# Kernel optimization log

Hardware: AMD Instinct MI355X
Metric: run time of the kernel (lower is better)

The kernel has to match this reference:

```python
import jax, jax.numpy as jnp
import numpy as np

N = 400_000      # total nodes in batched graph
E = 6_400_000    # total edges (avg degree 16)
G = 6_400        # total small graphs
B = 64           # samples; num[i] graphs per sample, sum(num)=G
F = 31           # feature dim (hard-coded in TAG)
K = 2            # TAGConv hops
L = 5            # number of TAGConv layers
MAXG = 120       # max graphs per sample (120*31 pad)


def setup_inputs() -> dict:
    key = jax.random.key(0)
    ks = jax.random.split(key, 8)
    x = jax.random.normal(ks[0], (N, F), dtype=jnp.float32)
    src = jax.random.randint(ks[1], (E,), 0, N, dtype=jnp.int32)
    dst = jax.random.randint(ks[2], (E,), 0, N, dtype=jnp.int32)
    # contiguous (sorted) graph assignment, every graph non-empty (~62 nodes each)
    graph_ids = jnp.asarray((np.arange(N, dtype=np.int64) * G) // N, dtype=jnp.int32)
    num = jnp.full((B,), G // B, dtype=jnp.int32)  # 100 graphs per sample
    Ws = jax.random.normal(ks[3], (L, (K + 1) * F, F), dtype=jnp.float32) * 0.1
    bs = jax.random.normal(ks[4], (L, F), dtype=jnp.float32) * 0.01
    w_gate = jax.random.normal(ks[5], (F,), dtype=jnp.float32) * 0.1
    b_gate = jax.random.normal(ks[6], (1,), dtype=jnp.float32) * 0.01
    return {"x": x, "Ws": Ws, "bs": bs, "w_gate": w_gate, "b_gate": b_gate,
            "src": src, "dst": dst, "graph_ids": graph_ids, "num": num}


def reference(x, Ws, bs, w_gate, b_gate, src, dst, graph_ids, num):
    # symmetric normalization: norm = in_deg^{-1/2}, deg clamped to >=1 (DGL TAGConv)
    deg = jax.ops.segment_sum(jnp.ones((E,), x.dtype), dst, num_segments=N)
    norm = jnp.clip(deg, 1.0, None) ** -0.5  # [N]

    def tagconv(h, W, b):
        fstack = [h]
        cur = h
        for _ in range(K):
            cur = norm[:, None] * cur
            cur = jax.ops.segment_sum(cur[src], dst, num_segments=N)  # SPMM hop
            cur = norm[:, None] * cur
            fstack.append(cur)
        return jnp.concatenate(fstack, axis=-1) @ W + b  # [N, F]

    h = x
    for l in range(L):
        h = jax.nn.relu(tagconv(h, Ws[l], bs[l]))

    # GlobalAttentionPooling: segment softmax over gate scores, weighted sum
    gate = h @ w_gate + b_gate[0]                                   # [N]
    gmax = jax.ops.segment_max(gate, graph_ids, num_segments=G)     # [G]
    e = jnp.exp(gate - gmax[graph_ids])
    den = jax.ops.segment_sum(e, graph_ids, num_segments=G)
    alpha = e / den[graph_ids]
    rep = jax.ops.segment_sum(alpha[:, None] * h, graph_ids, num_segments=G)  # [G, F]

    # split by num, flatten, pad to 120*31, stack
    csum = jnp.cumsum(num)
    offsets = jnp.concatenate([jnp.zeros((1,), jnp.int32), csum.astype(jnp.int32)])
    g = jnp.arange(G, dtype=jnp.int32)
    sample_id = jnp.searchsorted(csum, g, side="right").astype(jnp.int32)  # [G]
    pos = g - offsets[sample_id]
    out = jnp.zeros((B, MAXG, F), rep.dtype).at[sample_id, pos].set(rep)
    return out.reshape(B, MAXG * F)
```

## Files before the change

kernel.cpp:

```cpp
#include <hip/hip_runtime.h>
#include <hip/hip_bf16.h>

#define FDIM 31
#define FPAD 32
#define RSTRIDE 16

#define CBITS 11
#define CW    (1 << CBITS)
#define MAXBUK 256
#define TILE 4096

typedef int      iv4 __attribute__((ext_vector_type(4)));
typedef unsigned uv4 __attribute__((ext_vector_type(4)));

__device__ __forceinline__ float bf_lo(unsigned u) { return __uint_as_float(u << 16); }
__device__ __forceinline__ float bf_hi(unsigned u) { return __uint_as_float(u & 0xFFFF0000u); }
__device__ __forceinline__ unsigned pack2(float lo, float hi) {
    unsigned a = __float_as_uint(lo), b = __float_as_uint(hi);
    unsigned ra = (a + 0x7FFFu + ((a >> 16) & 1u)) >> 16;
    unsigned rb = (b + 0x7FFFu + ((b >> 16) & 1u)) >> 16;
    return ra | (rb << 16);
}

__device__ __forceinline__ int lb_gid(const int* __restrict__ gid, int Ntot, int g) {
    int lo = 0, hi = Ntot;
    while (lo < hi) { int mid = (lo + hi) >> 1; if (gid[mid] < g) lo = mid + 1; else hi = mid; }
    return lo;
}

__global__ __launch_bounds__(256) void multisplit_kernel(
    const int* __restrict__ src, const int* __restrict__ dst,
    int* __restrict__ gcnt, int* __restrict__ bucketed,
    int cap, int E, int nbuk)
{
    __shared__ int ordered[TILE];
    __shared__ int hist[MAXBUK];
    __shared__ int lofs[MAXBUK + 1];
    __shared__ int base_[MAXBUK];
    __shared__ int cur[MAXBUK];
    const int tid = threadIdx.x;
    const int e0 = blockIdx.x * TILE;
    const int n = min(TILE, E - e0);
    if (tid < MAXBUK) hist[tid] = 0;
    __syncthreads();
    for (int i = tid; i < n; i += 256)
        atomicAdd(&hist[dst[e0 + i] >> CBITS], 1);
    __syncthreads();
    if (tid == 0) {
        int a = 0;
        for (int b = 0; b < nbuk; ++b) { lofs[b] = a; a += hist[b]; }
        lofs[nbuk] = a;
    }
    __syncthreads();
    if (tid < nbuk) {
        int h = hist[tid];
        base_[tid] = h ? atomicAdd(&gcnt[tid], h) : 0;
        cur[tid] = lofs[tid];
    }
    __syncthreads();
    for (int i = tid; i < n; i += 256) {
        int s = src[e0 + i], d = dst[e0 + i];
        int b = d >> CBITS;
        int r = atomicAdd(&cur[b], 1);
        ordered[r] = (s << CBITS) | (d & (CW - 1));
    }
    __syncthreads();
    for (int i = tid; i < n; i += 256) {
        int lo = 0, hi = nbuk;
        while (hi - lo > 1) {
            int mid = (lo + hi) >> 1;
            if (lofs[mid] <= i) lo = mid; else hi = mid;
        }
        int b = lo;
        int pos = base_[b] + (i - lofs[b]);
        if (pos < cap) bucketed[(size_t)b * cap + pos] = ordered[i];
    }
}

__global__ void small_scans_kernel(const int* __restrict__ num, int* __restrict__ soff, int Bn,
                                   const int* __restrict__ gcnt, int* __restrict__ bbase,
                                   int nbuk, int cap) {
    if (threadIdx.x == 0 && blockIdx.x == 0) {
        int acc = 0; soff[0] = 0;
        for (int i = 0; i < Bn; ++i) { acc += num[i]; soff[i + 1] = acc; }
        int a = 0;
        for (int b = 0; b < nbuk; ++b) {
            bbase[b] = a;
            a += ((min(gcnt[b], cap) + 7) & ~7) + 7 * CW;
        }
    }
}

__global__ __launch_bounds__(1024) void bucket_build_kernel(
    const int* __restrict__ bucketed, const int* __restrict__ gcnt,
    const int* __restrict__ bbase,
    int* __restrict__ rowbeg, int* __restrict__ rowend,
    float* __restrict__ normv, float* __restrict__ invn,
    int* __restrict__ col,
    int cap, int N, int nbuk)
{
    __shared__ int hist[CW];
    __shared__ int lcur[CW];
    const int b = blockIdx.x, tid = threadIdx.x;
    hist[tid] = 0; hist[tid + 1024] = 0;
    __syncthreads();
    const int cnt = min(gcnt[b], cap);
    const int* reg = bucketed + (size_t)b * cap;
    for (int i = tid; i < cnt; i += 1024)
        atomicAdd(&hist[reg[i] & (CW - 1)], 1);
    __syncthreads();
    int c0 = hist[tid], c1 = hist[tid + 1024];
    int p0 = (c0 + 7) & ~7, p1 = (c1 + 7) & ~7;
    __syncthreads();
    hist[tid] = p0; hist[tid + 1024] = p1;
    __syncthreads();
    for (int off = 1; off < CW; off <<= 1) {
        int a0 = (tid >= off) ? hist[tid - off] : 0;
        int a1 = (tid + 1024 >= off) ? hist[tid + 1024 - off] : 0;
        __syncthreads();
        hist[tid] += a0; hist[tid + 1024] += a1;
        __syncthreads();
    }
    const int base = bbase[b];
    const int base_node = b << CBITS;
    int r0 = -1, r1 = -1;
    int node = base_node + tid;
    if (node < N) {
        r0 = base + hist[tid] - p0;
        rowbeg[node] = r0; rowend[node] = r0 + p0; lcur[tid] = r0;
        int cr = c0 > 0 ? c0 : 1;
        normv[node] = rsqrtf((float)cr);
        invn[node]  = sqrtf((float)cr);
    }
    node = base_node + tid + 1024;
    if (node < N) {
        r1 = base + hist[tid + 1024] - p1;
        rowbeg[node] = r1; rowend[node] = r1 + p1; lcur[tid + 1024] = r1;
        int cr = c1 > 0 ? c1 : 1;
        normv[node] = rsqrtf((float)cr);
        invn[node]  = sqrtf((float)cr);
    }
    __syncthreads();
    for (int i = tid; i < cnt; i += 1024) {
        int e = reg[i];
        int p = atomicAdd(&lcur[e & (CW - 1)], 1);
        col[p] = e >> CBITS;
    }
    if (r0 >= 0) for (int j = r0 + c0; j < r0 + p0; ++j) col[j] = N;
    if (r1 >= 0) for (int j = r1 + c1; j < r1 + p1; ++j) col[j] = N;
}

__global__ void cast_x_kernel(const float* __restrict__ x, const float* __restrict__ normv,
                              unsigned* __restrict__ A, int N) {
    int idx = blockIdx.x * 256 + threadIdx.x;
    if (idx >= (N + 1) * RSTRIDE) return;
    int n = idx >> 4, q = idx & 15;
    if (n >= N) { A[idx] = 0u; return; }
    float nv = normv[n];
    int f0 = 2 * q, f1 = 2 * q + 1;
    float lo = (f0 < FDIM) ? nv * x[(size_t)n * FDIM + f0] : 0.0f;
    float hi = (f1 < FDIM) ? nv * x[(size_t)n * FDIM + f1] : 0.0f;
    A[idx] = pack2(lo, hi);
}

#define GATHER8(HSRC, r0, r1, r2, r3, r4, r5, r6, r7, CA, CB)                    \
    r0 = *((const uint4*)(HSRC + (size_t)(CA).x * RSTRIDE) + sub);               \
    r1 = *((const uint4*)(HSRC + (size_t)(CA).y * RSTRIDE) + sub);               \
    r2 = *((const uint4*)(HSRC + (size_t)(CA).z * RSTRIDE) + sub);               \
    r3 = *((const uint4*)(HSRC + (size_t)(CA).w * RSTRIDE) + sub);               \
    r4 = *((const uint4*)(HSRC + (size_t)(CB).x * RSTRIDE) + sub);               \
    r5 = *((const uint4*)(HSRC + (size_t)(CB).y * RSTRIDE) + sub);               \
    r6 = *((const uint4*)(HSRC + (size_t)(CB).z * RSTRIDE) + sub);               \
    r7 = *((const uint4*)(HSRC + (size_t)(CB).w * RSTRIDE) + sub);

#define ACC_EDGE(vN)                                                   \
    acc0 += bf_lo(vN.x); acc1 += bf_hi(vN.x);                          \
    acc2 += bf_lo(vN.y); acc3 += bf_hi(vN.y);                          \
    acc4 += bf_lo(vN.z); acc5 += bf_hi(vN.z);                          \
    acc6 += bf_lo(vN.w); acc7 += bf_hi(vN.w);

#define ACC8(r0, r1, r2, r3, r4, r5, r6, r7)                           \
    ACC_EDGE(r0) ACC_EDGE(r1) ACC_EDGE(r2) ACC_EDGE(r3)                \
    ACC_EDGE(r4) ACC_EDGE(r5) ACC_EDGE(r6) ACC_EDGE(r7)

__global__ __launch_bounds__(256) void spmm_kernel(const unsigned* __restrict__ Hin,
                                                   unsigned* __restrict__ Hout,
                                                   const int* __restrict__ rowbeg,
                                                   const int* __restrict__ rowend,
                                                   const int* __restrict__ col,
                                                   const float* __restrict__ normv, int N) {
    int node = blockIdx.x * 64 + (threadIdx.x >> 2);
    int sub = threadIdx.x & 3;
    if (node > N) return;
    if (node == N) {
        uint4 z; z.x = z.y = z.z = z.w = 0u;
        *((uint4*)(Hout + (size_t)N * RSTRIDE) + sub) = z;
        return;
    }
    int s = rowbeg[node];
    int nit = (rowend[node] - s) >> 3;
    float acc0 = 0.f, acc1 = 0.f, acc2 = 0.f, acc3 = 0.f;
    float acc4 = 0.f, acc5 = 0.f, acc6 = 0.f, acc7 = 0.f;
    if (nit > 0) {
        const iv4* cl = (const iv4*)(col + s);
        iv4 ca = __builtin_nontemporal_load(cl);
        iv4 cb = __builtin_nontemporal_load(cl + 1);
        for (int it = 0; it < nit; ++it) {
            uint4 v0, v1, v2, v3, v4, v5, v6, v7;
            GATHER8(Hin, v0, v1, v2, v3, v4, v5, v6, v7, ca, cb)
            const iv4* nx = cl + ((it + 1 < nit) ? 2 : 0);
            iv4 na = __builtin_nontemporal_load(nx);
            iv4 nb = __builtin_nontemporal_load(nx + 1);
            cl += 2;
            ACC8(v0, v1, v2, v3, v4, v5, v6, v7)
            ca = na; cb = nb;
        }
    }
    float nv = normv[node];
    float nn2 = nv * nv;
    uint4 o;
    o.x = pack2(nn2 * acc0, nn2 * acc1);
    o.y = pack2(nn2 * acc2, nn2 * acc3);
    o.z = pack2(nn2 * acc4, nn2 * acc5);
    o.w = pack2(nn2 * acc6, nn2 * acc7);
    *((uint4*)(Hout + (size_t)node * RSTRIDE) + sub) = o;
}

template<int JB, int NJ>
__device__ __forceinline__ void mlp_pre(const uint4 (&ra)[4], const uint4 (&rb)[4],
                                        const float* __restrict__ W, float (&out)[8]) {
    const unsigned* ru = (const unsigned*)ra;
    const unsigned* rv = (const unsigned*)rb;
#pragma unroll
    for (int i = 0; i < FDIM; ++i) {
        float va = (i & 1) ? bf_hi(ru[i >> 1]) : bf_lo(ru[i >> 1]);
        float vb = (i & 1) ? bf_hi(rv[i >> 1]) : bf_lo(rv[i >> 1]);
#pragma unroll
        for (int jj = 0; jj < NJ; ++jj) {
            out[jj] = fmaf(va, W[i * FDIM + JB + jj], out[jj]);
            out[jj] = fmaf(vb, W[FDIM * FDIM + i * FDIM + JB + jj], out[jj]);
        }
    }
}

template<int JB, int NJ>
__device__ __forceinline__ void mlp_fin(float (&out)[8], const float* hp,
                                        const float* __restrict__ W,
                                        const float* __restrict__ bias,
                                        float inv, float sc, unsigned* orow,
                                        const float* __restrict__ w_gate,
                                        int do_gate, float& gp) {
#pragma unroll
    for (int i = 0; i < FDIM; ++i) {
        float v = hp[i];
#pragma unroll
        for (int jj = 0; jj < NJ; ++jj)
            out[jj] = fmaf(v, W[2 * FDIM * FDIM + i * FDIM + JB + jj], out[jj]);
    }
#pragma unroll
    for (int jj = 0; jj < NJ; ++jj)
        out[jj] = fmaxf(fmaf(out[jj], inv, bias[JB + jj]), 0.0f);
#pragma unroll
    for (int jj = NJ; jj < 8; ++jj) out[jj] = 0.0f;
    uint4 q;
    q.x = pack2(sc * out[0], sc * out[1]);
    q.y = pack2(sc * out[2], sc * out[3]);
    q.z = pack2(sc * out[4], sc * out[5]);
    q.w = pack2(sc * out[6], sc * out[7]);
    ((uint4*)orow)[JB >> 3] = q;
    if (do_gate) {
#pragma unroll
        for (int jj = 0; jj < NJ; ++jj)
            gp = fmaf(out[jj], w_gate[JB + jj], gp);
    }
}

__global__ __launch_bounds__(256, 4) void spmm_mlp_kernel(
    const unsigned* __restrict__ Hb,
    unsigned* __restrict__ Ha,
    const int* __restrict__ rowbeg,
    const int* __restrict__ rowend,
    const int* __restrict__ col,
    const float* __restrict__ normv,
    const float* __restrict__ invn,
    const float* __restrict__ W,
    const float* __restrict__ bias,
    float* __restrict__ gatev,
    const float* __restrict__ w_gate,
    const float* __restrict__ b_gate,
    int do_gate, int N)
{
    __shared__ float hcL[64 * 33];
    __shared__ float gred[256];
    const int tid = threadIdx.x;
    const int ln = tid & 63;
    const int wv = tid >> 6;
    const int n2 = blockIdx.x * 64 + ln;
    uint4 ra[4], rb[4];
    if (n2 < N) {
        const uint4* pa = (const uint4*)(Ha + (size_t)n2 * RSTRIDE);
        const uint4* pb = (const uint4*)(Hb + (size_t)n2 * RSTRIDE);
#pragma unroll
        for (int q = 0; q < 4; ++q) ra[q] = pa[q];
#pragma unroll
        for (int q = 0; q < 4; ++q) rb[q] = pb[q];
    }
    {
        int node = blockIdx.x * 64 + (tid >> 2);
        int sub = tid & 3;
        if (node < N) {
            int s = rowbeg[node];
            int nit = (rowend[node] - s) >> 3;
            float acc0 = 0.f, acc1 = 0.f, acc2 = 0.f, acc3 = 0.f;
            float acc4 = 0.f, acc5 = 0.f, acc6 = 0.f, acc7 = 0.f;
            if (nit > 0) {
                const iv4* cl = (const iv4*)(col + s);
                iv4 ca = __builtin_nontemporal_load(cl);
                iv4 cb = __builtin_nontemporal_load(cl + 1);
                for (int it = 0; it < nit; ++it) {
                    uint4 v0, v1, v2, v3, v4, v5, v6, v7;
                    GATHER8(Hb, v0, v1, v2, v3, v4, v5, v6, v7, ca, cb)
                    const iv4* nx = cl + ((it + 1 < nit) ? 2 : 0);
                    iv4 na = __builtin_nontemporal_load(nx);
                    iv4 nb = __builtin_nontemporal_load(nx + 1);
                    cl += 2;
                    ACC8(v0, v1, v2, v3, v4, v5, v6, v7)
                    ca = na; cb = nb;
                }
            }
            float nv = normv[node];
            float nn2 = nv * nv;
            float* hp = &hcL[(tid >> 2) * 33 + sub * 8];
            hp[0] = nn2 * acc0; hp[1] = nn2 * acc1;
            hp[2] = nn2 * acc2; hp[3] = nn2 * acc3;
            hp[4] = nn2 * acc4; hp[5] = nn2 * acc5;
            hp[6] = nn2 * acc6; hp[7] = nn2 * acc7;
        }
    }
    float out[8];
#pragma unroll
    for (int jj = 0; jj < 8; ++jj) out[jj] = 0.0f;
    if (n2 < N) {
        if      (wv == 0) mlp_pre<0,  8>(ra, rb, W, out);
        else if (wv == 1) mlp_pre<8,  8>(ra, rb, W, out);
        else if (wv == 2) mlp_pre<16, 8>(ra, rb, W, out);
        else              mlp_pre<24, 7>(ra, rb, W, out);
    }
    __syncthreads();
    float gp = 0.0f;
    if (n2 < N) {
        const float* hp = &hcL[ln * 33];
        float inv = invn[n2];
        float sc = do_gate ? 1.0f : normv[n2];
        unsigned* orow = Ha + (size_t)n2 * RSTRIDE;
        if      (wv == 0) mlp_fin<0,  8>(out, hp, W, bias, inv, sc, orow, w_gate, do_gate, gp);
        else if (wv == 1) mlp_fin<8,  8>(out, hp, W, bias, inv, sc, orow, w_gate, do_gate, gp);
        else if (wv == 2) mlp_fin<16, 8>(out, hp, W, bias, inv, sc, orow, w_gate, do_gate, gp);
        else              mlp_fin<24, 7>(out, hp, W, bias, inv, sc, orow, w_gate, do_gate, gp);
    }
    if (do_gate) {
        gred[tid] = gp;
        __syncthreads();
        if (tid < 64 && n2 < N)
            gatev[n2] = b_gate[0] + gred[tid] + gred[tid + 64] + gred[tid + 128] + gred[tid + 192];
    }
}


__global__ __launch_bounds__(64) void graph_reduce_kernel(const float* __restrict__ gate,
                                                          const int* __restrict__ gid,
                                                          const int* __restrict__ soff, int Bn,
                                                          int Ntot,
                                                          float* __restrict__ gmax,
                                                          float* __restrict__ gden) {
    int g = blockIdx.x;
    if (g >= soff[Bn]) return;
    int s = lb_gid(gid, Ntot, g), e = lb_gid(gid, Ntot, g + 1);
    float m = -1e30f;
    for (int n = s + threadIdx.x; n < e; n += 64) m = fmaxf(m, gate[n]);
#pragma unroll
    for (int o = 32; o > 0; o >>= 1) m = fmaxf(m, __shfl_xor(m, o));
    float d = 0.0f;
    for (int n = s + threadIdx.x; n < e; n += 64) d += expf(gate[n] - m);
#pragma unroll
    for (int o = 32; o > 0; o >>= 1) d += __shfl_xor(d, o);
    if (threadIdx.x == 0) { gmax[g] = m; gden[g] = d; }
}

__global__ __launch_bounds__(64) void rep_scatter_kernel(const unsigned short* __restrict__ H,
                                                         const float* __restrict__ gate,
                                                         const int* __restrict__ gid,
                                                         const int* __restrict__ soff,
                                                         int MAXG, int Ntot,
                                                         const float* __restrict__ gmax,
                                                         const float* __restrict__ gden,
                                                         float* __restrict__ out) {
    int s = blockIdx.x / MAXG;
    int pos = blockIdx.x % MAXG;
    int t = threadIdx.x;
    if (t >= FDIM) return;
    int gbeg = soff[s], gend = soff[s + 1];
    float* op = out + ((size_t)s * MAXG + pos) * FDIM + t;
    if (pos >= gend - gbeg) { *op = 0.0f; return; }
    int g = gbeg + pos;
    int ns = lb_gid(gid, Ntot, g), ne = lb_gid(gid, Ntot, g + 1);
    float m = gmax[g], den = gden[g];
    float acc = 0.0f;
    for (int n = ns; n < ne; ++n) {
        float hv = __uint_as_float((unsigned)H[(size_t)n * FPAD + t] << 16);
        acc += expf(gate[n] - m) * hv;
    }
    *op = acc / den;
}


extern "C" void kernel_launch(void* const* d_in, const int* in_sizes, int n_in,
                              void* d_out, int out_size, void* d_ws, size_t ws_size,
                              hipStream_t stream) {
    const float* x      = (const float*)d_in[0];
    const float* Ws     = (const float*)d_in[1];
    const float* bs     = (const float*)d_in[2];
    const float* w_gate = (const float*)d_in[3];
    const float* b_gate = (const float*)d_in[4];
    const int* src       = (const int*)d_in[5];
    const int* dst       = (const int*)d_in[6];
    const int* graph_ids = (const int*)d_in[7];
    const int* num       = (const int*)d_in[8];
    float* out  = (float*)d_out;

    const int N  = in_sizes[7];
    const int E  = in_sizes[5];
    const int Bn = in_sizes[8];
    const int F  = in_sizes[3];
    const int L  = in_sizes[2] / F;
    const int nW = in_sizes[1];
    const int WperL = nW / L;
    const int MAXG = out_size / (Bn * F);
    const int Gmax = Bn * MAXG;

    const int nbuk = (N + CW - 1) / CW;
    const int cap  = E / nbuk + E / (8 * nbuk) + 2048;

    char* p = (char*)d_ws;
    auto alloc = [&](size_t bytes) {
        void* r = (void*)p;
        p += (bytes + 255) & ~(size_t)255;
        return r;
    };
    unsigned* HA = (unsigned*)alloc((size_t)(N + 1) * RSTRIDE * 4);
    unsigned* HB = (unsigned*)alloc((size_t)(N + 1) * RSTRIDE * 4);
    int*   colw  = (int*)alloc(((size_t)E + (size_t)nbuk * (7 * CW + 16)) * 4);
    int*   bkt   = (int*)alloc((size_t)nbuk * cap * 4);
    int*   gcnt  = (int*)alloc((size_t)nbuk * 4);
    int*   bbase = (int*)alloc((size_t)nbuk * 4);
    int*   rowb  = (int*)alloc((size_t)(N + 1) * 4);
    int*   rowe  = (int*)alloc((size_t)(N + 1) * 4);
    float* normv = (float*)alloc((size_t)N * 4);
    float* invnv = (float*)alloc((size_t)N * 4);
    float* gatev = (float*)alloc((size_t)N * 4);
    float* gmax  = (float*)alloc((size_t)Gmax * 4);
    float* gden  = (float*)alloc((size_t)Gmax * 4);
    int*   soff  = (int*)alloc((size_t)(Bn + 1) * 4);

    (void)hipMemsetAsync(gcnt, 0, (size_t)nbuk * 4, stream);

    const int NT = (E + TILE - 1) / TILE;
    multisplit_kernel<<<NT, 256, 0, stream>>>(src, dst, gcnt, bkt, cap, E, nbuk);
    small_scans_kernel<<<1, 64, 0, stream>>>(num, soff, Bn, gcnt, bbase, nbuk, cap);
    bucket_build_kernel<<<nbuk, 1024, 0, stream>>>(bkt, gcnt, bbase, rowb, rowe,
                                                   normv, invnv, colw, cap, N, nbuk);

    cast_x_kernel<<<((N + 1) * RSTRIDE + 255) / 256, 256, 0, stream>>>(x, normv, HA, N);

    const int SB  = (N + 1 + 63) / 64;
    const int SB2 = (N + 63) / 64;
    for (int l = 0; l < L; ++l) {
        spmm_kernel<<<SB, 256, 0, stream>>>(HA, HB, rowb, rowe, colw, normv, N);
        spmm_mlp_kernel<<<SB2, 256, 0, stream>>>(HB, HA, rowb, rowe, colw, normv, invnv,
                                                 Ws + (size_t)l * WperL, bs + (size_t)l * F,
                                                 gatev, w_gate, b_gate,
                                                 (l == L - 1) ? 1 : 0, N);
    }

    graph_reduce_kernel<<<Gmax, 64, 0, stream>>>(gatev, graph_ids, soff, Bn, N, gmax, gden);
    rep_scatter_kernel<<<Gmax, 64, 0, stream>>>((const unsigned short*)HA, gatev, graph_ids,
                                                soff, MAXG, N, gmax, gden, out);
    (void)n_in; (void)ws_size;
}
```

Measured before the change: 1.556 ms.

## Fuse cast into bucket build, merge pooling kernels, simplify multisplit and scans

Several preprocessing changes land together. The multisplit kernel now writes edges straight to global buckets through per-bucket atomics, without the shared-memory staging reorder. The small scans use a wave-parallel shuffle scan. The x-to-bf16 cast is folded into bucket_build, and the two pooling kernels merge into one, with the padded output zeroed by a memset. Together these cut kernel launches and intermediate traffic, but the direct bucket writes are less coalesced.

```diff
diff --git a/kernel.cpp b/kernel.cpp
--- a/kernel.cpp
+++ b/kernel.cpp
@@ -33,10 +33,7 @@
     int* __restrict__ gcnt, int* __restrict__ bucketed,
     int cap, int E, int nbuk)
 {
-    __shared__ int ordered[TILE];
     __shared__ int hist[MAXBUK];
-    __shared__ int lofs[MAXBUK + 1];
-    __shared__ int base_[MAXBUK];
     __shared__ int cur[MAXBUK];
     const int tid = threadIdx.x;
     const int e0 = blockIdx.x * TILE;
@@ -46,48 +43,49 @@
     for (int i = tid; i < n; i += 256)
         atomicAdd(&hist[dst[e0 + i] >> CBITS], 1);
     __syncthreads();
-    if (tid == 0) {
-        int a = 0;
-        for (int b = 0; b < nbuk; ++b) { lofs[b] = a; a += hist[b]; }
-        lofs[nbuk] = a;
-    }
-    __syncthreads();
     if (tid < nbuk) {
         int h = hist[tid];
-        base_[tid] = h ? atomicAdd(&gcnt[tid], h) : 0;
-        cur[tid] = lofs[tid];
+        cur[tid] = h ? atomicAdd(&gcnt[tid], h) : 0;
     }
     __syncthreads();
     for (int i = tid; i < n; i += 256) {
         int s = src[e0 + i], d = dst[e0 + i];
         int b = d >> CBITS;
-        int r = atomicAdd(&cur[b], 1);
-        ordered[r] = (s << CBITS) | (d & (CW - 1));
-    }
-    __syncthreads();
-    for (int i = tid; i < n; i += 256) {
-        int lo = 0, hi = nbuk;
-        while (hi - lo > 1) {
-            int mid = (lo + hi) >> 1;
-            if (lofs[mid] <= i) lo = mid; else hi = mid;
-        }
-        int b = lo;
-        int pos = base_[b] + (i - lofs[b]);
-        if (pos < cap) bucketed[(size_t)b * cap + pos] = ordered[i];
-    }
-}
-
-__global__ void small_scans_kernel(const int* __restrict__ num, int* __restrict__ soff, int Bn,
-                                   const int* __restrict__ gcnt, int* __restrict__ bbase,
-                                   int nbuk, int cap) {
-    if (threadIdx.x == 0 && blockIdx.x == 0) {
-        int acc = 0; soff[0] = 0;
-        for (int i = 0; i < Bn; ++i) { acc += num[i]; soff[i + 1] = acc; }
-        int a = 0;
-        for (int b = 0; b < nbuk; ++b) {
-            bbase[b] = a;
-            a += ((min(gcnt[b], cap) + 7) & ~7) + 7 * CW;
-        }
+        int pos = atomicAdd(&cur[b], 1);
+        if (pos < cap) bucketed[(size_t)b * cap + pos] = (s << CBITS) | (d & (CW - 1));
+    }
+}
+
+__global__ __launch_bounds__(64) void small_scans_kernel(
+    const int* __restrict__ num, int* __restrict__ soff, int Bn,
+    const int* __restrict__ gcnt, int* __restrict__ bbase, int nbuk, int cap) {
+    const int t = threadIdx.x;
+    __shared__ int carry;
+    if (t == 0) { carry = 0; soff[0] = 0; }
+    __syncthreads();
+    for (int c0 = 0; c0 < Bn; c0 += 64) {
+        int idx = c0 + t;
+        int v = (idx < Bn) ? num[idx] : 0;
+        int sc = v;
+#pragma unroll
+        for (int o = 1; o < 64; o <<= 1) { int u = __shfl_up(sc, o); if (t >= o) sc += u; }
+        if (idx < Bn) soff[idx + 1] = carry + sc;
+        __syncthreads();
+        if (t == 63) carry += sc;
+        __syncthreads();
+    }
+    if (t == 0) carry = 0;
+    __syncthreads();
+    for (int c0 = 0; c0 < nbuk; c0 += 64) {
+        int idx = c0 + t;
+        int v = (idx < nbuk) ? (((min(gcnt[idx], cap) + 7) & ~7) + 7 * CW) : 0;
+        int sc = v;
+#pragma unroll
+        for (int o = 1; o < 64; o <<= 1) { int u = __shfl_up(sc, o); if (t >= o) sc += u; }
+        if (idx < nbuk) bbase[idx] = carry + sc - v;
+        __syncthreads();
+        if (t == 63) carry += sc;
+        __syncthreads();
     }
 }
 
@@ -97,10 +95,12 @@
     int* __restrict__ rowbeg, int* __restrict__ rowend,
     float* __restrict__ normv, float* __restrict__ invn,
     int* __restrict__ col,
+    const float* __restrict__ x, unsigned* __restrict__ HA,
     int cap, int N, int nbuk)
 {
     __shared__ int hist[CW];
     __shared__ int lcur[CW];
+    __shared__ float nvL[CW];
     const int b = blockIdx.x, tid = threadIdx.x;
     hist[tid] = 0; hist[tid + 1024] = 0;
     __syncthreads();
@@ -129,7 +129,8 @@
         r0 = base + hist[tid] - p0;
         rowbeg[node] = r0; rowend[node] = r0 + p0; lcur[tid] = r0;
         int cr = c0 > 0 ? c0 : 1;
-        normv[node] = rsqrtf((float)cr);
+        float nv = rsqrtf((float)cr);
+        normv[node] = nv; nvL[tid] = nv;
         invn[node]  = sqrtf((float)cr);
     }
     node = base_node + tid + 1024;
@@ -137,7 +138,8 @@
         r1 = base + hist[tid + 1024] - p1;
         rowbeg[node] = r1; rowend[node] = r1 + p1; lcur[tid + 1024] = r1;
         int cr = c1 > 0 ? c1 : 1;
-        normv[node] = rsqrtf((float)cr);
+        float nv = rsqrtf((float)cr);
+        normv[node] = nv; nvL[tid + 1024] = nv;
         invn[node]  = sqrtf((float)cr);
     }
     __syncthreads();
@@ -148,19 +150,23 @@
     }
     if (r0 >= 0) for (int j = r0 + c0; j < r0 + p0; ++j) col[j] = N;
     if (r1 >= 0) for (int j = r1 + c1; j < r1 + p1; ++j) col[j] = N;
-}
-
-__global__ void cast_x_kernel(const float* __restrict__ x, const float* __restrict__ normv,
-                              unsigned* __restrict__ A, int N) {
-    int idx = blockIdx.x * 256 + threadIdx.x;
-    if (idx >= (N + 1) * RSTRIDE) return;
-    int n = idx >> 4, q = idx & 15;
-    if (n >= N) { A[idx] = 0u; return; }
-    float nv = normv[n];
-    int f0 = 2 * q, f1 = 2 * q + 1;
-    float lo = (f0 < FDIM) ? nv * x[(size_t)n * FDIM + f0] : 0.0f;
-    float hi = (f1 < FDIM) ? nv * x[(size_t)n * FDIM + f1] : 0.0f;
-    A[idx] = pack2(lo, hi);
+    __syncthreads();
+    const int nodes_here = min(CW, N + 1 - base_node);
+    for (int idx = tid; idx < nodes_here * RSTRIDE; idx += 1024) {
+        int loc = idx >> 4, q = idx & 15;
+        int nodec = base_node + loc;
+        unsigned val = 0u;
+        if (nodec < N) {
+            float nv = nvL[loc];
+            int f0 = 2 * q, f1 = 2 * q + 1;
+            float lo = (f0 < FDIM) ? nv * x[(size_t)nodec * FDIM + f0] : 0.0f;
+            float hi = (f1 < FDIM) ? nv * x[(size_t)nodec * FDIM + f1] : 0.0f;
+            val = pack2(lo, hi);
+        }
+        HA[(size_t)nodec * RSTRIDE + q] = val;
+    }
+    if (b == nbuk - 1 && base_node + CW <= N)
+        for (int q = tid; q < RSTRIDE; q += 1024) HA[(size_t)N * RSTRIDE + q] = 0u;
 }
 
 #define GATHER8(HSRC, r0, r1, r2, r3, r4, r5, r6, r7, CA, CB)                    \
@@ -366,51 +372,32 @@
     }
 }
 
-
-__global__ __launch_bounds__(64) void graph_reduce_kernel(const float* __restrict__ gate,
-                                                          const int* __restrict__ gid,
-                                                          const int* __restrict__ soff, int Bn,
-                                                          int Ntot,
-                                                          float* __restrict__ gmax,
-                                                          float* __restrict__ gden) {
+__global__ __launch_bounds__(64) void gpool_kernel(const unsigned short* __restrict__ H,
+                                                   const float* __restrict__ gate,
+                                                   const int* __restrict__ gid,
+                                                   const int* __restrict__ soff,
+                                                   int Bn, int MAXG, int Ntot,
+                                                   float* __restrict__ out) {
     int g = blockIdx.x;
     if (g >= soff[Bn]) return;
+    int t = threadIdx.x;
     int s = lb_gid(gid, Ntot, g), e = lb_gid(gid, Ntot, g + 1);
     float m = -1e30f;
-    for (int n = s + threadIdx.x; n < e; n += 64) m = fmaxf(m, gate[n]);
+    for (int n = s + t; n < e; n += 64) m = fmaxf(m, gate[n]);
 #pragma unroll
     for (int o = 32; o > 0; o >>= 1) m = fmaxf(m, __shfl_xor(m, o));
     float d = 0.0f;
-    for (int n = s + threadIdx.x; n < e; n += 64) d += expf(gate[n] - m);
+    for (int n = s + t; n < e; n += 64) d += expf(gate[n] - m);
 #pragma unroll
     for (int o = 32; o > 0; o >>= 1) d += __shfl_xor(d, o);
-    if (threadIdx.x == 0) { gmax[g] = m; gden[g] = d; }
-}
-
-__global__ __launch_bounds__(64) void rep_scatter_kernel(const unsigned short* __restrict__ H,
-                                                         const float* __restrict__ gate,
-                                                         const int* __restrict__ gid,
-                                                         const int* __restrict__ soff,
-                                                         int MAXG, int Ntot,
-                                                         const float* __restrict__ gmax,
-                                                         const float* __restrict__ gden,
-                                                         float* __restrict__ out) {
-    int s = blockIdx.x / MAXG;
-    int pos = blockIdx.x % MAXG;
-    int t = threadIdx.x;
+    int lo = 0, hi = Bn;
+    while (hi - lo > 1) { int mid = (lo + hi) >> 1; if (soff[mid] <= g) lo = mid; else hi = mid; }
+    int smp = lo, pos = g - soff[smp];
     if (t >= FDIM) return;
-    int gbeg = soff[s], gend = soff[s + 1];
-    float* op = out + ((size_t)s * MAXG + pos) * FDIM + t;
-    if (pos >= gend - gbeg) { *op = 0.0f; return; }
-    int g = gbeg + pos;
-    int ns = lb_gid(gid, Ntot, g), ne = lb_gid(gid, Ntot, g + 1);
-    float m = gmax[g], den = gden[g];
     float acc = 0.0f;
-    for (int n = ns; n < ne; ++n) {
-        float hv = __uint_as_float((unsigned)H[(size_t)n * FPAD + t] << 16);
-        acc += expf(gate[n] - m) * hv;
-    }
-    *op = acc / den;
+    for (int n = s; n < e; ++n)
+        acc += expf(gate[n] - m) * __uint_as_float((unsigned)H[(size_t)n * FPAD + t] << 16);
+    out[((size_t)smp * MAXG + pos) * FDIM + t] = acc / d;
 }
 
 
@@ -458,19 +445,17 @@
     float* normv = (float*)alloc((size_t)N * 4);
     float* invnv = (float*)alloc((size_t)N * 4);
     float* gatev = (float*)alloc((size_t)N * 4);
-    float* gmax  = (float*)alloc((size_t)Gmax * 4);
-    float* gden  = (float*)alloc((size_t)Gmax * 4);
     int*   soff  = (int*)alloc((size_t)(Bn + 1) * 4);
 
     (void)hipMemsetAsync(gcnt, 0, (size_t)nbuk * 4, stream);
+    (void)hipMemsetAsync(out, 0, (size_t)out_size * 4, stream);
 
     const int NT = (E + TILE - 1) / TILE;
     multisplit_kernel<<<NT, 256, 0, stream>>>(src, dst, gcnt, bkt, cap, E, nbuk);
     small_scans_kernel<<<1, 64, 0, stream>>>(num, soff, Bn, gcnt, bbase, nbuk, cap);
     bucket_build_kernel<<<nbuk, 1024, 0, stream>>>(bkt, gcnt, bbase, rowb, rowe,
-                                                   normv, invnv, colw, cap, N, nbuk);
-
-    cast_x_kernel<<<((N + 1) * RSTRIDE + 255) / 256, 256, 0, stream>>>(x, normv, HA, N);
+                                                   normv, invnv, colw, x, HA,
+                                                   cap, N, nbuk);
 
     const int SB  = (N + 1 + 63) / 64;
     const int SB2 = (N + 63) / 64;
@@ -482,8 +467,7 @@
                                                  (l == L - 1) ? 1 : 0, N);
     }
 
-    graph_reduce_kernel<<<Gmax, 64, 0, stream>>>(gatev, graph_ids, soff, Bn, N, gmax, gden);
-    rep_scatter_kernel<<<Gmax, 64, 0, stream>>>((const unsigned short*)HA, gatev, graph_ids,
-                                                soff, MAXG, N, gmax, gden, out);
+    gpool_kernel<<<Gmax, 64, 0, stream>>>((const unsigned short*)HA, gatev, graph_ids,
+                                          soff, Bn, MAXG, N, out);
     (void)n_in; (void)ws_size;
 }
```

Result: slower. 1.603 ms (+3.0%).
